# Performance work log

Measured on AMD Instinct MI355X. Metric: run time of the kernel, lower is better.

## Reference

```python
import jax, jax.numpy as jnp
import numpy as np

N_HEAD, DK, DV = 16, 64, 64
TEMP = DK ** 0.5
LN_EPS = 1e-5


def setup_inputs() -> dict:
    key = jax.random.key(0)
    ks = jax.random.split(key, 8)
    B, LQ, LK = 8, 1024, 1024
    D1, D2 = 768, 1024
    return {
        'q': jax.random.normal(ks[0], (B, LQ, D1), jnp.float32),
        'k': jax.random.normal(ks[1], (B, LK, D2), jnp.float32),
        'v': jax.random.normal(ks[2], (B, LK, D2), jnp.float32),
        'w_qs': jax.random.normal(ks[3], (D1, N_HEAD * DK), jnp.float32) * 0.02,
        'w_ks': jax.random.normal(ks[4], (D2, N_HEAD * DK), jnp.float32) * 0.02,
        'w_vs': jax.random.normal(ks[5], (D2, N_HEAD * DV), jnp.float32) * 0.02,
        'fc_w': jax.random.normal(ks[6], (N_HEAD * DV, D2), jnp.float32) * 0.02,
        'resid_w': jax.random.normal(ks[7], (D1, N_HEAD * DV), jnp.float32) * 0.02,
        'resid_b': jnp.zeros((N_HEAD * DV,), jnp.float32),
        'ln_gamma': jnp.ones((D2,), jnp.float32),
        'ln_beta': jnp.zeros((D2,), jnp.float32),
    }


def reference(q, k, v, w_qs, w_ks, w_vs, fc_w, resid_w, resid_b, ln_gamma, ln_beta):
    B, LQ, _ = q.shape
    LK = k.shape[1]
    residual = q
    # project and split heads: [B, L, H, d] -> [B, H, L, d]
    Q = (q @ w_qs).reshape(B, LQ, N_HEAD, DK).transpose(0, 2, 1, 3)
    K = (k @ w_ks).reshape(B, LK, N_HEAD, DK).transpose(0, 2, 1, 3)
    V = (v @ w_vs).reshape(B, LK, N_HEAD, DV).transpose(0, 2, 1, 3)
    scores = jnp.einsum('bhqd,bhkd->bhqk', Q / TEMP, K)
    p = jax.nn.softmax(scores, axis=-1)
    # reverse-complement attention (RCA): reverse=True
    p = (1.0 - p) / (LK - 1)
    out = jnp.einsum('bhqk,bhkd->bhqd', p, V)  # dropout is eval-mode identity
    out = out.transpose(0, 2, 1, 3).reshape(B, LQ, N_HEAD * DV)
    out = out @ fc_w
    out = out + (residual @ resid_w + resid_b)
    mean = jnp.mean(out, axis=-1, keepdims=True)
    var = jnp.var(out, axis=-1, keepdims=True)
    out = (out - mean) * jax.lax.rsqrt(var + LN_EPS) * ln_gamma + ln_beta
    return out  # relu=False
```

## Files before the change

kernel.cpp:

```cpp
#include <hip/hip_runtime.h>

typedef __bf16 bf16_t;
typedef __bf16 bf16x8 __attribute__((ext_vector_type(8)));
typedef __bf16 bf16x4 __attribute__((ext_vector_type(4)));
typedef float  f32x4  __attribute__((ext_vector_type(4)));
typedef short  short4v __attribute__((ext_vector_type(4)));

#if __has_builtin(__builtin_amdgcn_exp2f)
#define EXP2(x) __builtin_amdgcn_exp2f(x)
#else
#define EXP2(x) exp2f(x)
#endif

#define DEVFN __device__ __forceinline__

DEVFN void gl_lds16(void* lds_base, const void* gsrc) {
  __builtin_amdgcn_global_load_lds(
      (const __attribute__((address_space(1))) void*)gsrc,
      (__attribute__((address_space(3))) void*)lds_base, 16, 0, 0);
}

__global__ __launch_bounds__(256) void k_convert_all(
    const float* __restrict__ q, const float* __restrict__ k, const float* __restrict__ v,
    bf16_t* __restrict__ qb, bf16_t* __restrict__ kb, bf16_t* __restrict__ vb,
    float* __restrict__ Vs) {
  if (blockIdx.x == 0) {
    for (int j = threadIdx.x; j < 8192; j += 256) Vs[j] = 0.f;
  }
  const int NQ = 1572864, NK = 2097152, NT = NQ + 2 * NK;
  int stride = gridDim.x * 256;
  for (int i = blockIdx.x * 256 + threadIdx.x; i < NT; i += stride) {
    const float* src; bf16_t* dst; int off;
    if (i < NQ)           { src = q; dst = qb; off = i; }
    else if (i < NQ + NK) { src = k; dst = kb; off = i - NQ; }
    else                  { src = v; dst = vb; off = i - NQ - NK; }
    float4 vv = reinterpret_cast<const float4*>(src)[off];
    bf16x4 o;
    o[0] = (bf16_t)vv.x; o[1] = (bf16_t)vv.y; o[2] = (bf16_t)vv.z; o[3] = (bf16_t)vv.w;
    reinterpret_cast<bf16x4*>(dst)[off] = o;
  }
}

__global__ __launch_bounds__(256) void k_transpose_all(
    const float* __restrict__ w_qs, const float* __restrict__ w_ks,
    const float* __restrict__ w_vs, const float* __restrict__ fc_w,
    const float* __restrict__ resid_w,
    bf16_t* __restrict__ wqsT, bf16_t* __restrict__ wksT, bf16_t* __restrict__ wvsT,
    bf16_t* __restrict__ fcwT, bf16_t* __restrict__ rswT) {
  int bid = blockIdx.x;
  const float* w; bf16_t* wt; int K;
  if (bid < 192)      { w = w_qs;    wt = wqsT; K = 768; }
  else if (bid < 448) { w = w_ks;    wt = wksT; K = 1024; bid -= 192; }
  else if (bid < 704) { w = w_vs;    wt = wvsT; K = 1024; bid -= 448; }
  else if (bid < 960) { w = fc_w;    wt = fcwT; K = 1024; bid -= 704; }
  else                { w = resid_w; wt = rswT; K = 768;  bid -= 960; }
  __shared__ float t[64][65];
  const int bk = (bid >> 4) << 6;
  const int bn = (bid & 15) << 6;
  const int rr = threadIdx.x >> 4;
  const int cc = (threadIdx.x & 15) << 2;
#pragma unroll
  for (int i = 0; i < 4; ++i) {
    int r = i * 16 + rr;
    float4 v = *reinterpret_cast<const float4*>(&w[(size_t)(bk + r) * 1024 + bn + cc]);
    t[r][cc] = v.x; t[r][cc + 1] = v.y; t[r][cc + 2] = v.z; t[r][cc + 3] = v.w;
  }
  __syncthreads();
#pragma unroll
  for (int i = 0; i < 4; ++i) {
    int n = i * 16 + rr;
    bf16x4 o;
    o[0] = (bf16_t)t[cc][n];     o[1] = (bf16_t)t[cc + 1][n];
    o[2] = (bf16_t)t[cc + 2][n]; o[3] = (bf16_t)t[cc + 3][n];
    *reinterpret_cast<bf16x4*>(&wt[(size_t)(bn + n) * K + bk + cc]) = o;
  }
}

__global__ __launch_bounds__(256) void k_transpose_v(
    const bf16_t* __restrict__ Vp, bf16_t* __restrict__ Vt, float* __restrict__ Vs) {
  const int kt = blockIdx.x & 15;
  const int bh = blockIdx.x >> 4;
  const int b = bh >> 4, h = bh & 15;
  __shared__ unsigned short t[64][72];
  __shared__ float red[4][64];
#pragma unroll
  for (int i = 0; i < 2; ++i) {
    int cid = i * 256 + threadIdx.x;
    int r = cid >> 3, c = (cid & 7) * 8;
    uint4 v = *reinterpret_cast<const uint4*>(
        Vp + ((size_t)(b * 1024 + kt * 64 + r)) * 1024 + h * 64 + c);
    const unsigned short* pv = reinterpret_cast<const unsigned short*>(&v);
#pragma unroll
    for (int j = 0; j < 8; ++j) t[r][c + j] = pv[j];
  }
  __syncthreads();
#pragma unroll
  for (int i = 0; i < 2; ++i) {
    int cid = i * 256 + threadIdx.x;
    int d = cid >> 3, c = (cid & 7) * 8;
    unsigned short tmp[8];
#pragma unroll
    for (int j = 0; j < 8; ++j) tmp[j] = t[c + j][d];
    uint4 w = *reinterpret_cast<uint4*>(tmp);
    if ((d >> 3) & 1) {
      unsigned tx = w.x, ty = w.y;
      w.x = w.z; w.y = w.w; w.z = tx; w.w = ty;
    }
    char* dst = (char*)Vt + ((size_t)(bh * 16 + kt)) * 8192 + d * 128 +
                ((((c >> 3) ^ (d & 7))) << 4);
    *reinterpret_cast<uint4*>(dst) = w;
  }
  const int d = threadIdx.x & 63, seg = threadIdx.x >> 6;
  float s = 0.f;
#pragma unroll
  for (int i = 0; i < 16; ++i)
    s += (float)*(const bf16_t*)&t[seg * 16 + i][d];
  red[seg][d] = s;
  __syncthreads();
  if (threadIdx.x < 64)
    atomicAdd(&Vs[bh * 64 + threadIdx.x],
              red[0][threadIdx.x] + red[1][threadIdx.x] + red[2][threadIdx.x] + red[3][threadIdx.x]);
}

__global__ __launch_bounds__(256) void k_gemm_bt(
    const bf16_t* __restrict__ A, const bf16_t* __restrict__ Bt,
    bf16_t* __restrict__ C, int N, int K, float oscale) {
  __shared__ bf16_t sm[4][4096];
  const int bpx = gridDim.x >> 3;
  const int wg = (blockIdx.x & 7) * bpx + (blockIdx.x >> 3);
  const int tn = N >> 7;
  const int m0 = (wg / tn) << 7;
  const int n0 = (wg % tn) << 7;
  const int lane = threadIdx.x & 63;
  const int wv = threadIdx.x >> 6;
  const int wr = (wv >> 1) * 64, wc = (wv & 1) * 64;
  const int lr = lane & 15, lk = lane >> 4;
  const int so0 = wv * 2048 + lane * 16;
  const int so1 = so0 + 1024;
  const int r0 = so0 >> 6, c0 = so0 & 63;
  const int r1 = so1 >> 6, c1 = so1 & 63;
  const char* Apc = (const char*)A;
  const char* Btc = (const char*)Bt;
  f32x4 zro = {0.f, 0.f, 0.f, 0.f};
  f32x4 acc[4][4];
#pragma unroll
  for (int i = 0; i < 4; ++i)
#pragma unroll
    for (int j = 0; j < 4; ++j) acc[i][j] = zro;

  const int nk = K >> 5;
  auto stage = [&](int buf, int t) {
    gl_lds16((char*)sm[buf] + wv * 2048,        Apc + ((size_t)(m0 + r0) * K + t * 32) * 2 + c0);
    gl_lds16((char*)sm[buf] + wv * 2048 + 1024, Apc + ((size_t)(m0 + r1) * K + t * 32) * 2 + c1);
    gl_lds16((char*)sm[2 + buf] + wv * 2048,        Btc + ((size_t)(n0 + r0) * K + t * 32) * 2 + c0);
    gl_lds16((char*)sm[2 + buf] + wv * 2048 + 1024, Btc + ((size_t)(n0 + r1) * K + t * 32) * 2 + c1);
  };
  stage(0, 0);
  __syncthreads();
  for (int t = 0; t < nk; ++t) {
    const int cur = t & 1;
    if (t + 1 < nk) stage(cur ^ 1, t + 1);
    const char* AsB = (const char*)sm[cur];
    const char* BsB = (const char*)sm[2 + cur];
    bf16x8 af[4], bfr[4];
#pragma unroll
    for (int i = 0; i < 4; ++i)
      af[i] = *(const bf16x8*)(AsB + (wr + i * 16 + lr) * 64 + lk * 16);
#pragma unroll
    for (int j = 0; j < 4; ++j)
      bfr[j] = *(const bf16x8*)(BsB + (wc + j * 16 + lr) * 64 + lk * 16);
#pragma unroll
    for (int i = 0; i < 4; ++i)
#pragma unroll
      for (int j = 0; j < 4; ++j)
        acc[i][j] = __builtin_amdgcn_mfma_f32_16x16x32_bf16(af[i], bfr[j], acc[i][j], 0, 0, 0);
    __syncthreads();
  }
#pragma unroll
  for (int i = 0; i < 4; ++i)
#pragma unroll
    for (int j = 0; j < 4; ++j)
#pragma unroll
      for (int r = 0; r < 4; ++r)
        C[(size_t)(m0 + wr + i * 16 + lk * 4 + r) * N + n0 + wc + j * 16 + lr] =
            (bf16_t)(acc[i][j][r] * oscale);
}

__global__ __launch_bounds__(256) void k_gemm_final(
    const bf16_t* __restrict__ A1, const bf16_t* __restrict__ B1t, int K1,
    const bf16_t* __restrict__ A2, const bf16_t* __restrict__ B2t, int K2,
    const float* __restrict__ bias, float* __restrict__ Y, int N) {
  __shared__ bf16_t sm[4][4096];
  const int bpx = gridDim.x >> 3;
  const int wg = (blockIdx.x & 7) * bpx + (blockIdx.x >> 3);
  const int tn = N >> 7;
  const int m0 = (wg / tn) << 7;
  const int n0 = (wg % tn) << 7;
  const int lane = threadIdx.x & 63;
  const int wv = threadIdx.x >> 6;
  const int wr = (wv >> 1) * 64, wc = (wv & 1) * 64;
  const int lr = lane & 15, lk = lane >> 4;
  const int so0 = wv * 2048 + lane * 16;
  const int so1 = so0 + 1024;
  const int r0 = so0 >> 6, c0 = so0 & 63;
  const int r1 = so1 >> 6, c1 = so1 & 63;
  f32x4 zro = {0.f, 0.f, 0.f, 0.f};
  f32x4 acc[4][4];
#pragma unroll
  for (int i = 0; i < 4; ++i)
#pragma unroll
    for (int j = 0; j < 4; ++j) acc[i][j] = zro;

  const bf16_t* Ap[2] = {A1, A2};
  const bf16_t* Bp[2] = {B1t, B2t};
  const int Kp_[2] = {K1, K2};
  for (int ph = 0; ph < 2; ++ph) {
    const char* Apc = (const char*)Ap[ph];
    const char* Btc = (const char*)Bp[ph];
    const int K = Kp_[ph];
    const int nk = K >> 5;
    auto stage = [&](int buf, int t) {
      gl_lds16((char*)sm[buf] + wv * 2048,        Apc + ((size_t)(m0 + r0) * K + t * 32) * 2 + c0);
      gl_lds16((char*)sm[buf] + wv * 2048 + 1024, Apc + ((size_t)(m0 + r1) * K + t * 32) * 2 + c1);
      gl_lds16((char*)sm[2 + buf] + wv * 2048,        Btc + ((size_t)(n0 + r0) * K + t * 32) * 2 + c0);
      gl_lds16((char*)sm[2 + buf] + wv * 2048 + 1024, Btc + ((size_t)(n0 + r1) * K + t * 32) * 2 + c1);
    };
    stage(0, 0);
    __syncthreads();
    for (int t = 0; t < nk; ++t) {
      const int cur = t & 1;
      if (t + 1 < nk) stage(cur ^ 1, t + 1);
      const char* AsB = (const char*)sm[cur];
      const char* BsB = (const char*)sm[2 + cur];
      bf16x8 af[4], bfr[4];
#pragma unroll
      for (int i = 0; i < 4; ++i)
        af[i] = *(const bf16x8*)(AsB + (wr + i * 16 + lr) * 64 + lk * 16);
#pragma unroll
      for (int j = 0; j < 4; ++j)
        bfr[j] = *(const bf16x8*)(BsB + (wc + j * 16 + lr) * 64 + lk * 16);
#pragma unroll
      for (int i = 0; i < 4; ++i)
#pragma unroll
        for (int j = 0; j < 4; ++j)
          acc[i][j] = __builtin_amdgcn_mfma_f32_16x16x32_bf16(af[i], bfr[j], acc[i][j], 0, 0, 0);
      __syncthreads();
    }
  }
#pragma unroll
  for (int i = 0; i < 4; ++i)
#pragma unroll
    for (int j = 0; j < 4; ++j) {
      float bv = bias[n0 + wc + j * 16 + lr];
#pragma unroll
      for (int r = 0; r < 4; ++r)
        Y[(size_t)(m0 + wr + i * 16 + lk * 4 + r) * N + n0 + wc + j * 16 + lr] =
            acc[i][j][r] + bv;
    }
}

__global__ __launch_bounds__(256) void k_attn(
    const bf16_t* __restrict__ Qp, const bf16_t* __restrict__ Kp,
    const bf16_t* __restrict__ Vt, const float* __restrict__ Vsum,
    bf16_t* __restrict__ Aout) {
  const int bid = blockIdx.x;
  const int wgid = (bid & 7) * 128 + (bid >> 3);
  const int qg = wgid & 7;
  const int bh = wgid >> 3;
  const int b = bh >> 4, h = bh & 15;
  __shared__ bf16_t Ks[2][64 * 64];
  __shared__ bf16_t Vs[2][64 * 64];
  const int lane = threadIdx.x & 63;
  const int wv = threadIdx.x >> 6;
  const int lr = lane & 15, lk = lane >> 4;

  const int o0 = wv * 2048 + lane * 16;
  const int o1 = o0 + 1024;
  const int row0 = o0 >> 7, row1 = o1 >> 7;
  const int sc0 = ((((o0 >> 4) & 7) ^ (row0 & 7)) << 4);
  const int sc1 = ((((o1 >> 4) & 7) ^ (row1 & 7)) << 4);

  const char* Ksrc0 = (const char*)(Kp + ((size_t)(b * 1024 + row0)) * 1024 + h * 64) + sc0;
  const char* Ksrc1 = (const char*)(Kp + ((size_t)(b * 1024 + row1)) * 1024 + h * 64) + sc1;
  const char* Vtile = (const char*)Vt + (size_t)bh * 131072 + o0;

  gl_lds16((char*)&Ks[0][0] + o0, Ksrc0);
  gl_lds16((char*)&Ks[0][0] + o1, Ksrc1);
  gl_lds16((char*)&Vs[0][0] + o0, Vtile);
  gl_lds16((char*)&Vs[0][0] + o1, Vtile + 1024);

  bf16x8 qa[2][2];
#pragma unroll
  for (int st = 0; st < 2; ++st) {
    const char* qsrc =
        (const char*)(Qp + ((size_t)(b * 1024 + qg * 128 + st * 64 + wv * 16 + lr)) * 1024 + h * 64);
    qa[st][0] = *(const bf16x8*)(qsrc + lk * 16);
    qa[st][1] = *(const bf16x8*)(qsrc + 64 + lk * 16);
  }
  __syncthreads();

  const int kb0 = lr * 128 + ((lk ^ (lr & 7)) << 4);
  const int kb1 = lr * 128 + (((4 + lk) ^ (lr & 7)) << 4);
  const int vbase = lr * 128 + (((lk & 1) ^ (lr >> 3)) << 3);
  int gsw[4];
#pragma unroll
  for (int g = 0; g < 4; ++g)
    gsw[g] = (((2 * g + (lk >> 1)) ^ (lr & 7)) << 4);

  f32x4 zro = {0.f, 0.f, 0.f, 0.f};
  f32x4 oacc[2][4];
  f32x4 sum[2];
#pragma unroll
  for (int st = 0; st < 2; ++st) {
    sum[st] = zro;
#pragma unroll
    for (int g = 0; g < 4; ++g) oacc[st][g] = zro;
  }
  const short4v ones = {(short)0x3F80, (short)0x3F80, (short)0x3F80, (short)0x3F80};

  for (int kt = 0; kt < 16; ++kt) {
    const int cur = kt & 1;
    const char* KsB = (const char*)&Ks[cur][0];
    const char* VsB = (const char*)&Vs[cur][0];
    if (kt < 15) {
      char* KsN = (char*)&Ks[cur ^ 1][0];
      char* VsN = (char*)&Vs[cur ^ 1][0];
      const size_t koff = (size_t)(kt + 1) * 131072;
      const size_t voff = (size_t)(kt + 1) * 8192;
      gl_lds16(KsN + o0, Ksrc0 + koff);
      gl_lds16(KsN + o1, Ksrc1 + koff);
      gl_lds16(VsN + o0, Vtile + voff);
      gl_lds16(VsN + o1, Vtile + voff + 1024);
    }

    f32x4 sacc[2][4];
#pragma unroll
    for (int st = 0; st < 2; ++st)
#pragma unroll
      for (int g = 0; g < 4; ++g) sacc[st][g] = zro;
    {
      bf16x8 kf[4];
#pragma unroll
      for (int g = 0; g < 4; ++g) kf[g] = *(const bf16x8*)(KsB + kb0 + g * 2048);
#pragma unroll
      for (int st = 0; st < 2; ++st)
#pragma unroll
        for (int g = 0; g < 4; ++g)
          sacc[st][g] = __builtin_amdgcn_mfma_f32_16x16x32_bf16(kf[g], qa[st][0], sacc[st][g], 0, 0, 0);
#pragma unroll
      for (int g = 0; g < 4; ++g) kf[g] = *(const bf16x8*)(KsB + kb1 + g * 2048);
#pragma unroll
      for (int st = 0; st < 2; ++st)
#pragma unroll
        for (int g = 0; g < 4; ++g)
          sacc[st][g] = __builtin_amdgcn_mfma_f32_16x16x32_bf16(kf[g], qa[st][1], sacc[st][g], 0, 0, 0);
    }

    short4v pa[2][4];
#pragma unroll
    for (int st = 0; st < 2; ++st)
#pragma unroll
      for (int g = 0; g < 4; ++g) {
        bf16x4 pw;
#pragma unroll
        for (int r = 0; r < 4; ++r) pw[r] = (bf16_t)EXP2(sacc[st][g][r]);
        pa[st][g] = __builtin_bit_cast(short4v, pw);
      }

#pragma unroll
    for (int g = 0; g < 4; ++g) {
      short4v vbv[4];
#pragma unroll
      for (int gd = 0; gd < 4; ++gd)
        vbv[gd] = *(const short4v*)(VsB + vbase + gsw[g] + gd * 2048);
#pragma unroll
      for (int st = 0; st < 2; ++st) {
        sum[st] = __builtin_amdgcn_mfma_f32_16x16x16bf16_1k(pa[st][g], ones, sum[st], 0, 0, 0);
#pragma unroll
        for (int gd = 0; gd < 4; ++gd)
          oacc[st][gd] = __builtin_amdgcn_mfma_f32_16x16x16bf16_1k(pa[st][g], vbv[gd], oacc[st][gd], 0, 0, 0);
      }
    }
    __syncthreads();
  }

  float vs_d[4];
#pragma unroll
  for (int gd = 0; gd < 4; ++gd) vs_d[gd] = Vsum[bh * 64 + gd * 16 + lr];
#pragma unroll
  for (int st = 0; st < 2; ++st) {
    float inv[4];
#pragma unroll
    for (int r = 0; r < 4; ++r) inv[r] = 1.0f / sum[st][r];
#pragma unroll
    for (int gd = 0; gd < 4; ++gd)
#pragma unroll
      for (int r = 0; r < 4; ++r) {
        int d = gd * 16 + lr;
        int qrow = qg * 128 + st * 64 + wv * 16 + lk * 4 + r;
        float attnv = oacc[st][gd][r] * inv[r];
        float val = (vs_d[gd] - attnv) * (1.0f / 1023.0f);
        Aout[((size_t)(b * 1024 + qrow)) * 1024 + h * 64 + d] = (bf16_t)val;
      }
  }
}

__global__ __launch_bounds__(256) void k_ln(
    const float* __restrict__ Y, const float* __restrict__ gamma,
    const float* __restrict__ beta, float* __restrict__ out) {
  const int row = blockIdx.x, tid = threadIdx.x;
  const float4 x = reinterpret_cast<const float4*>(Y + (size_t)row * 1024)[tid];
  float s = x.x + x.y + x.z + x.w;
  float q = x.x * x.x + x.y * x.y + x.z * x.z + x.w * x.w;
#pragma unroll
  for (int off = 32; off > 0; off >>= 1) {
    s += __shfl_xor(s, off, 64);
    q += __shfl_xor(q, off, 64);
  }
  __shared__ float ss[4], qs[4];
  if ((tid & 63) == 0) { ss[tid >> 6] = s; qs[tid >> 6] = q; }
  __syncthreads();
  s = ss[0] + ss[1] + ss[2] + ss[3];
  q = qs[0] + qs[1] + qs[2] + qs[3];
  float mean = s * (1.f / 1024.f);
  float var = q * (1.f / 1024.f) - mean * mean;
  float rstd = rsqrtf(var + 1e-5f);
  float4 g = reinterpret_cast<const float4*>(gamma)[tid];
  float4 bt = reinterpret_cast<const float4*>(beta)[tid];
  float4 o;
  o.x = (x.x - mean) * rstd * g.x + bt.x;
  o.y = (x.y - mean) * rstd * g.y + bt.y;
  o.z = (x.z - mean) * rstd * g.z + bt.z;
  o.w = (x.w - mean) * rstd * g.w + bt.w;
  reinterpret_cast<float4*>(out + (size_t)row * 1024)[tid] = o;
}

extern "C" void kernel_launch(void* const* d_in, const int* in_sizes, int n_in,
                              void* d_out, int out_size, void* d_ws, size_t ws_size,
                              hipStream_t stream) {
  (void)in_sizes; (void)n_in; (void)out_size;
  const float* q       = (const float*)d_in[0];
  const float* k       = (const float*)d_in[1];
  const float* v       = (const float*)d_in[2];
  const float* w_qs    = (const float*)d_in[3];
  const float* w_ks    = (const float*)d_in[4];
  const float* w_vs    = (const float*)d_in[5];
  const float* fc_w    = (const float*)d_in[6];
  const float* resid_w = (const float*)d_in[7];
  const float* resid_b = (const float*)d_in[8];
  const float* ln_g    = (const float*)d_in[9];
  const float* ln_b    = (const float*)d_in[10];
  float* out = (float*)d_out;
  char* ws = (char*)d_ws;

  if (ws_size < (size_t)122716160) return;

  bf16_t* qb   = (bf16_t*)(ws + 0);
  bf16_t* kb   = (bf16_t*)(ws + 12582912);
  bf16_t* vb   = (bf16_t*)(ws + 29360128);
  float*  Y    = (float*)(ws + 12582912);
  bf16_t* wqsT = (bf16_t*)(ws + 46137344);
  bf16_t* wksT = (bf16_t*)(ws + 47710208);
  bf16_t* wvsT = (bf16_t*)(ws + 49807360);
  bf16_t* fcwT = (bf16_t*)(ws + 51904512);
  bf16_t* rswT = (bf16_t*)(ws + 54001664);
  bf16_t* Qp   = (bf16_t*)(ws + 55574528);
  bf16_t* Kp   = (bf16_t*)(ws + 72351744);
  bf16_t* Vp   = (bf16_t*)(ws + 89128960);
  bf16_t* Aout = (bf16_t*)(ws + 89128960);
  bf16_t* VtT  = (bf16_t*)(ws + 105906176);
  float*  Vsm  = (float*)(ws + 122683392);

  k_convert_all<<<2048, 256, 0, stream>>>(q, k, v, qb, kb, vb, Vsm);
  k_transpose_all<<<1152, 256, 0, stream>>>(w_qs, w_ks, w_vs, fc_w, resid_w,
                                            wqsT, wksT, wvsT, fcwT, rswT);
  k_gemm_bt<<<512, 256, 0, stream>>>(qb, wqsT, Qp, 1024, 768, 0.18033688011f);
  k_gemm_bt<<<512, 256, 0, stream>>>(kb, wksT, Kp, 1024, 1024, 1.0f);
  k_gemm_bt<<<512, 256, 0, stream>>>(vb, wvsT, Vp, 1024, 1024, 1.0f);
  k_transpose_v<<<2048, 256, 0, stream>>>(Vp, VtT, Vsm);
  k_attn<<<1024, 256, 0, stream>>>(Qp, Kp, VtT, Vsm, Aout);
  k_gemm_final<<<512, 256, 0, stream>>>(Aout, fcwT, 1024, qb, rswT, 768, resid_b, Y, 1024);
  k_ln<<<8192, 256, 0, stream>>>(Y, ln_g, ln_b, out);
}
```

Before: 205.7 us.

## Merge QKV projection GEMMs into one launch and use K=32 MFMA for PV

Replaces the three separate projection GEMM launches with a single 1536-block kernel that routes each block to the Q, K or V projection. This removes launch gaps and tail underutilisation between them. In attention, the PV product and the row-sum now use the 16x16x32 bf16 MFMA instead of 16x16x16. That halves the instruction count, and the V fragments are read as 8-wide loads. To match the new P register layout, the V transpose swizzle is simplified and the K tile rows are permuted at load time.

```diff
diff --git a/kernel.cpp b/kernel.cpp
--- a/kernel.cpp
+++ b/kernel.cpp
@@ -4,7 +4,6 @@
 typedef __bf16 bf16x8 __attribute__((ext_vector_type(8)));
 typedef __bf16 bf16x4 __attribute__((ext_vector_type(4)));
 typedef float  f32x4  __attribute__((ext_vector_type(4)));
-typedef short  short4v __attribute__((ext_vector_type(4)));
 
 #if __has_builtin(__builtin_amdgcn_exp2f)
 #define EXP2(x) __builtin_amdgcn_exp2f(x)
@@ -101,14 +100,9 @@
     unsigned short tmp[8];
 #pragma unroll
     for (int j = 0; j < 8; ++j) tmp[j] = t[c + j][d];
-    uint4 w = *reinterpret_cast<uint4*>(tmp);
-    if ((d >> 3) & 1) {
-      unsigned tx = w.x, ty = w.y;
-      w.x = w.z; w.y = w.w; w.z = tx; w.w = ty;
-    }
     char* dst = (char*)Vt + ((size_t)(bh * 16 + kt)) * 8192 + d * 128 +
                 ((((c >> 3) ^ (d & 7))) << 4);
-    *reinterpret_cast<uint4*>(dst) = w;
+    *reinterpret_cast<uint4*>(dst) = *reinterpret_cast<uint4*>(tmp);
   }
   const int d = threadIdx.x & 63, seg = threadIdx.x >> 6;
   float s = 0.f;
@@ -122,12 +116,9 @@
               red[0][threadIdx.x] + red[1][threadIdx.x] + red[2][threadIdx.x] + red[3][threadIdx.x]);
 }
 
-__global__ __launch_bounds__(256) void k_gemm_bt(
-    const bf16_t* __restrict__ A, const bf16_t* __restrict__ Bt,
-    bf16_t* __restrict__ C, int N, int K, float oscale) {
-  __shared__ bf16_t sm[4][4096];
-  const int bpx = gridDim.x >> 3;
-  const int wg = (blockIdx.x & 7) * bpx + (blockIdx.x >> 3);
+DEVFN void gemm_core(const bf16_t* __restrict__ A, const bf16_t* __restrict__ Bt,
+                     bf16_t* __restrict__ C, int N, int K, float oscale,
+                     int wg, bf16_t (*sm)[4096]) {
   const int tn = N >> 7;
   const int m0 = (wg / tn) << 7;
   const int n0 = (wg % tn) << 7;
@@ -184,6 +175,21 @@
       for (int r = 0; r < 4; ++r)
         C[(size_t)(m0 + wr + i * 16 + lk * 4 + r) * N + n0 + wc + j * 16 + lr] =
             (bf16_t)(acc[i][j][r] * oscale);
+}
+
+__global__ __launch_bounds__(256) void k_gemm_proj(
+    const bf16_t* __restrict__ qb, const bf16_t* __restrict__ wqsT, bf16_t* __restrict__ Qp,
+    const bf16_t* __restrict__ kb, const bf16_t* __restrict__ wksT, bf16_t* __restrict__ Kp,
+    const bf16_t* __restrict__ vb, const bf16_t* __restrict__ wvsT, bf16_t* __restrict__ Vp,
+    float qscale) {
+  __shared__ bf16_t sm[4][4096];
+  const int bid = blockIdx.x;
+  const int route = bid >> 9;
+  const int sbid = bid & 511;
+  const int wg = (sbid & 7) * 64 + (sbid >> 3);
+  if (route == 0)      gemm_core(qb, wqsT, Qp, 1024, 768,  qscale, wg, sm);
+  else if (route == 1) gemm_core(kb, wksT, Kp, 1024, 1024, 1.0f,   wg, sm);
+  else                 gemm_core(vb, wvsT, Vp, 1024, 1024, 1.0f,   wg, sm);
 }
 
 __global__ __launch_bounds__(256) void k_gemm_final(
@@ -279,9 +285,11 @@
   const int row0 = o0 >> 7, row1 = o1 >> 7;
   const int sc0 = ((((o0 >> 4) & 7) ^ (row0 & 7)) << 4);
   const int sc1 = ((((o1 >> 4) & 7) ^ (row1 & 7)) << 4);
-
-  const char* Ksrc0 = (const char*)(Kp + ((size_t)(b * 1024 + row0)) * 1024 + h * 64) + sc0;
-  const char* Ksrc1 = (const char*)(Kp + ((size_t)(b * 1024 + row1)) * 1024 + h * 64) + sc1;
+  const int srow0 = (row0 & 0x23) | ((row0 & 0x0C) << 1) | ((row0 & 0x10) >> 2);
+  const int srow1 = (row1 & 0x23) | ((row1 & 0x0C) << 1) | ((row1 & 0x10) >> 2);
+
+  const char* Ksrc0 = (const char*)(Kp + ((size_t)(b * 1024 + srow0)) * 1024 + h * 64) + sc0;
+  const char* Ksrc1 = (const char*)(Kp + ((size_t)(b * 1024 + srow1)) * 1024 + h * 64) + sc1;
   const char* Vtile = (const char*)Vt + (size_t)bh * 131072 + o0;
 
   gl_lds16((char*)&Ks[0][0] + o0, Ksrc0);
@@ -301,11 +309,8 @@
 
   const int kb0 = lr * 128 + ((lk ^ (lr & 7)) << 4);
   const int kb1 = lr * 128 + (((4 + lk) ^ (lr & 7)) << 4);
-  const int vbase = lr * 128 + (((lk & 1) ^ (lr >> 3)) << 3);
-  int gsw[4];
-#pragma unroll
-  for (int g = 0; g < 4; ++g)
-    gsw[g] = (((2 * g + (lk >> 1)) ^ (lr & 7)) << 4);
+  const int vsw0 = lr * 128 + (((0 + lk) ^ (lr & 7)) << 4);
+  const int vsw1 = lr * 128 + (((4 + lk) ^ (lr & 7)) << 4);
 
   f32x4 zro = {0.f, 0.f, 0.f, 0.f};
   f32x4 oacc[2][4];
@@ -316,7 +321,9 @@
 #pragma unroll
     for (int g = 0; g < 4; ++g) oacc[st][g] = zro;
   }
-  const short4v ones = {(short)0x3F80, (short)0x3F80, (short)0x3F80, (short)0x3F80};
+  bf16x8 ones8;
+#pragma unroll
+  for (int j = 0; j < 8; ++j) ones8[j] = (bf16_t)1.0f;
 
   for (int kt = 0; kt < 16; ++kt) {
     const int cur = kt & 1;
@@ -356,29 +363,33 @@
           sacc[st][g] = __builtin_amdgcn_mfma_f32_16x16x32_bf16(kf[g], qa[st][1], sacc[st][g], 0, 0, 0);
     }
 
-    short4v pa[2][4];
+    bf16x8 pa[2][2];
 #pragma unroll
     for (int st = 0; st < 2; ++st)
 #pragma unroll
-      for (int g = 0; g < 4; ++g) {
-        bf16x4 pw;
-#pragma unroll
-        for (int r = 0; r < 4; ++r) pw[r] = (bf16_t)EXP2(sacc[st][g][r]);
-        pa[st][g] = __builtin_bit_cast(short4v, pw);
+      for (int c = 0; c < 2; ++c) {
+        bf16x8 pw;
+#pragma unroll
+        for (int r = 0; r < 4; ++r) {
+          pw[r]     = (bf16_t)EXP2(sacc[st][2 * c][r]);
+          pw[4 + r] = (bf16_t)EXP2(sacc[st][2 * c + 1][r]);
+        }
+        pa[st][c] = pw;
       }
 
 #pragma unroll
-    for (int g = 0; g < 4; ++g) {
-      short4v vbv[4];
+    for (int c = 0; c < 2; ++c) {
+      const int vb = (c == 0) ? vsw0 : vsw1;
+      bf16x8 vf[4];
 #pragma unroll
       for (int gd = 0; gd < 4; ++gd)
-        vbv[gd] = *(const short4v*)(VsB + vbase + gsw[g] + gd * 2048);
+        vf[gd] = *(const bf16x8*)(VsB + vb + gd * 2048);
 #pragma unroll
       for (int st = 0; st < 2; ++st) {
-        sum[st] = __builtin_amdgcn_mfma_f32_16x16x16bf16_1k(pa[st][g], ones, sum[st], 0, 0, 0);
+        sum[st] = __builtin_amdgcn_mfma_f32_16x16x32_bf16(pa[st][c], ones8, sum[st], 0, 0, 0);
 #pragma unroll
         for (int gd = 0; gd < 4; ++gd)
-          oacc[st][gd] = __builtin_amdgcn_mfma_f32_16x16x16bf16_1k(pa[st][g], vbv[gd], oacc[st][gd], 0, 0, 0);
+          oacc[st][gd] = __builtin_amdgcn_mfma_f32_16x16x32_bf16(pa[st][c], vf[gd], oacc[st][gd], 0, 0, 0);
       }
     }
     __syncthreads();
@@ -474,9 +485,8 @@
   k_convert_all<<<2048, 256, 0, stream>>>(q, k, v, qb, kb, vb, Vsm);
   k_transpose_all<<<1152, 256, 0, stream>>>(w_qs, w_ks, w_vs, fc_w, resid_w,
                                             wqsT, wksT, wvsT, fcwT, rswT);
-  k_gemm_bt<<<512, 256, 0, stream>>>(qb, wqsT, Qp, 1024, 768, 0.18033688011f);
-  k_gemm_bt<<<512, 256, 0, stream>>>(kb, wksT, Kp, 1024, 1024, 1.0f);
-  k_gemm_bt<<<512, 256, 0, stream>>>(vb, wvsT, Vp, 1024, 1024, 1.0f);
+  k_gemm_proj<<<1536, 256, 0, stream>>>(qb, wqsT, Qp, kb, wksT, Kp, vb, wvsT, Vp,
+                                        0.18033688011f);
   k_transpose_v<<<2048, 256, 0, stream>>>(Vp, VtT, Vsm);
   k_attn<<<1024, 256, 0, stream>>>(Qp, Kp, VtT, Vsm, Aout);
   k_gemm_final<<<512, 256, 0, stream>>>(Aout, fcwT, 1024, qb, rswT, 768, resid_b, Y, 1024);
```

New measurement: 198.3 us. 3.6% less time.
